# Optimization experiments

Measured on AMD Instinct MI355X. Metric: run time of the kernel, lower is better.

Reference implementation:

```python
import jax, jax.numpy as jnp
import numpy as np

B, L, HS, WS = 4, 5, 32, 32
C = 256            # dim == heads * dim_head
M, D = 8, 32       # heads, dim_head
T, R = 2, 4        # num_types, num_relations
I = M * D          # inner_dim
EPS = 1e-5


def setup_inputs() -> dict:
    key = jax.random.key(0)
    ks = jax.random.split(key, 12)
    w = 0.02
    x = jax.random.normal(ks[0], (B, L, HS, WS, C), dtype=jnp.float32)
    mask = jnp.ones((B, HS, WS, L, L), dtype=jnp.int32)
    prior_encoding = jax.random.randint(ks[1], (B, L, HS, WS, 3), 0, T).astype(jnp.float32)
    return {
        "x": x,
        "mask": mask,
        "prior_encoding": prior_encoding,
        "ln_w": jnp.ones((C,), jnp.float32),
        "ln_b": jnp.zeros((C,), jnp.float32),
        "Wq": jax.random.normal(ks[2], (T, C, I), jnp.float32) * w,
        "bq": jnp.zeros((T, I), jnp.float32),
        "Wk": jax.random.normal(ks[3], (T, C, I), jnp.float32) * w,
        "bk": jnp.zeros((T, I), jnp.float32),
        "Wv": jax.random.normal(ks[4], (T, C, I), jnp.float32) * w,
        "bv": jnp.zeros((T, I), jnp.float32),
        "Wa": jax.random.normal(ks[5], (T, I, C), jnp.float32) * w,
        "ba": jnp.zeros((T, C), jnp.float32),
        "rel_att": jax.random.normal(ks[6], (R, M, D, D), jnp.float32) * w,
        "rel_msg": jax.random.normal(ks[7], (R, M, D, D), jnp.float32) * w,
    }


def _hgt_forward(x, mask, prior_encoding, ln_w, ln_b, Wq, bq, Wk, bk, Wv, bv, Wa, ba, rel_att, rel_msg):
    # pre-LayerNorm over channel dim
    mu = jnp.mean(x, axis=-1, keepdims=True)
    var = jnp.mean(jnp.square(x - mu), axis=-1, keepdims=True)
    xn = (x - mu) * jax.lax.rsqrt(var + EPS) * ln_w + ln_b

    # [B,L,H,W,C] -> [B,H,W,L,C]
    xp = jnp.transpose(xn, (0, 2, 3, 1, 4))
    types = prior_encoding[:, :, 0, 0, 2].astype(jnp.int32)  # [B,L]

    # per-type q/k/v projections via gather of type-indexed weights
    q = jnp.einsum('bhwlc,blci->bhwli', xp, Wq[types]) + bq[types][:, None, None]
    k = jnp.einsum('bhwlc,blci->bhwli', xp, Wk[types]) + bk[types][:, None, None]
    v = jnp.einsum('bhwlc,blci->bhwli', xp, Wv[types]) + bv[types][:, None, None]

    def to_heads(t):  # [B,H,W,L,I] -> [B,M,H,W,L,D]
        return jnp.transpose(t.reshape(B, HS, WS, L, M, D), (0, 4, 1, 2, 3, 5))
    q, k, v = to_heads(q), to_heads(k), to_heads(v)

    # relation-indexed edge weights: e_type = t_i * T + t_j
    e = types[:, :, None] * T + types[:, None, :]              # [B,L,L]
    w_att = jnp.transpose(rel_att[e], (0, 3, 1, 2, 4, 5))      # [B,M,L,L,D,D]
    w_msg = jnp.transpose(rel_msg[e], (0, 3, 1, 2, 4, 5))

    scale = D ** -0.5
    q_w = jnp.einsum('bmhwip,bmijpq->bmhwijq', q, w_att)
    att = jnp.einsum('bmhwijq,bmhwjq->bmhwij', q_w, k) * scale
    att = jnp.where(mask[:, None] == 0, -1e9, att)
    att = jax.nn.softmax(att, axis=-1)

    v_msg = jnp.einsum('bmijpc,bmhwjp->bmhwijc', w_msg, v)
    out = jnp.einsum('bmhwij,bmhwijc->bmhwic', att, v_msg)

    # [B,M,H,W,L,D] -> [B,H,W,L,C]
    out = jnp.transpose(out, (0, 2, 3, 4, 1, 5)).reshape(B, HS, WS, L, I)
    out = jnp.einsum('bhwli,blic->bhwlc', out, Wa[types]) + ba[types][:, None, None]
    # dropout is identity at inference
    return jnp.transpose(out, (0, 3, 1, 2, 4))                 # [B,L,H,W,C]


def reference(x, mask, prior_encoding, ln_w, ln_b, Wq, bq, Wk, bk, Wv, bv, Wa, ba, rel_att, rel_msg):
    return _hgt_forward(x, mask, prior_encoding, ln_w, ln_b, Wq, bq, Wk, bk, Wv, bv, Wa, ba, rel_att, rel_msg)
```

## Files before the change

### kernel.cpp

```cpp
#include <hip/hip_runtime.h>
#include <hip/hip_bf16.h>
#include <math.h>

#define BB 4
#define LL 5
#define HSZ 32
#define WSZ 32
#define PP (HSZ*WSZ)
#define CC 256
#define MM 8
#define DD 32
#define II 256
#define TT 2
#define NTOK (BB*PP*LL*II)
#define TILE_ELEMS 8192
#define SCALE 0.17677669529663687f

typedef short bf16x8 __attribute__((ext_vector_type(8)));
typedef float f32x4 __attribute__((ext_vector_type(4)));

static __device__ __forceinline__ ushort f2bf(float f) {
    unsigned u = __float_as_uint(f);
    unsigned r = (u + 0x7fffu + ((u >> 16) & 1u)) >> 16;
    return (ushort)r;
}
static __device__ __forceinline__ float bf2f(ushort u) {
    return __uint_as_float(((unsigned)u) << 16);
}

__global__ __launch_bounds__(256) void k_fold(
    const float* __restrict__ Wq, const float* __restrict__ Wv,
    const float* __restrict__ Wk, const float* __restrict__ Wa,
    const float* __restrict__ bq, const float* __restrict__ bv,
    const float* __restrict__ rel_att, const float* __restrict__ rel_msg,
    const float* __restrict__ x,
    const float* __restrict__ lnw, const float* __restrict__ lnb,
    ushort* __restrict__ packW, float* __restrict__ bEff,
    ushort* __restrict__ xnPack)
{
    __shared__ float As[1024];
    __shared__ ushort Apack[8192];
    const int blk = blockIdx.x;
    const int tid = threadIdx.x;

    if (blk < 64) {
        const int p  = blk >> 5;
        const int t  = (blk >> 4) & 1;
        const int ts = (blk >> 3) & 1;
        const int m  = blk & 7;
        const float* A = (p == 0)
            ? rel_att + (size_t)((t * 2 + ts) * 8 + m) * 1024
            : rel_msg + (size_t)((ts * 2 + t) * 8 + m) * 1024;
        for (int i = tid; i < 1024; i += 256) As[i] = A[i];
        __syncthreads();

        const float* W = ((p == 0) ? Wq : Wv) + (size_t)t * 65536;
        const int k = tid;
        float wrow[32];
        #pragma unroll
        for (int u = 0; u < 8; ++u)
            *(float4*)&wrow[u * 4] = *(const float4*)&W[k * 256 + m * 32 + u * 4];

        const int slot = (p == 0 ? 0 : 4) + t * 2 + ts;
        ushort* base = packW + (size_t)slot * 65536;
        const int kt = k >> 5, j = k & 7, lq = ((k >> 3) & 3) * 16;
        #pragma unroll
        for (int q = 0; q < 32; ++q) {
            float acc = 0.f;
            #pragma unroll
            for (int pp = 0; pp < 32; ++pp) acc += wrow[pp] * As[pp * 32 + q];
            const int nt = m * 2 + (q >> 4);
            const int lane = lq + (q & 15);
            base[(size_t)((nt * 8 + kt) * 64 + lane) * 8 + j] = f2bf(acc);
        }
        if (tid < 32) {
            const int q = tid;
            const float* bi = ((p == 0) ? bq : bv) + t * 256 + m * 32;
            float acc = 0.f;
            #pragma unroll
            for (int pp = 0; pp < 32; ++pp) acc += bi[pp] * As[pp * 32 + q];
            bEff[(p ? 1024 : 0) + (t * 2 + ts) * 256 + m * 32 + q] = acc;
        }
    } else if (blk < 192) {
        const int idx = blk - 64;
        const int which = idx >> 6;
        const int gi = (idx & 63) * 256 + tid;
        const int t = gi >> 13;
        const int sub = gi & 8191;
        const float* src = ((which == 0) ? Wk : Wa) + (size_t)t * 65536;
        const int slot = (which == 0 ? 8 : 10) + t;
        const int nt = sub >> 9, kt = (sub >> 6) & 7, lane = sub & 63;
        const int k0 = kt * 32 + (lane >> 4) * 8;
        const int n  = nt * 16 + (lane & 15);
        ushort h[8];
        #pragma unroll
        for (int j = 0; j < 8; ++j) h[j] = f2bf(src[(size_t)(k0 + j) * 256 + n]);
        uint4 o;
        o.x = (unsigned)h[0] | ((unsigned)h[1] << 16);
        o.y = (unsigned)h[2] | ((unsigned)h[3] << 16);
        o.z = (unsigned)h[4] | ((unsigned)h[5] << 16);
        o.w = (unsigned)h[6] | ((unsigned)h[7] << 16);
        *(uint4*)(packW + (size_t)slot * 65536 + (size_t)sub * 8) = o;
    } else {
        const int lblk = blk - 192;
        const int bl  = lblk >> 5;
        const int pt  = lblk & 31;
        const int p0  = pt * 32;

        const int r  = tid >> 3;
        const int jj = tid & 7;
        const float* xrow = x + ((size_t)bl * PP + p0 + r) * CC;
        float4 xv[8];
        float s1 = 0.f, s2 = 0.f;
        #pragma unroll
        for (int u = 0; u < 8; ++u) {
            xv[u] = *(const float4*)(xrow + jj * 32 + u * 4);
            s1 += xv[u].x + xv[u].y + xv[u].z + xv[u].w;
            s2 += xv[u].x * xv[u].x + xv[u].y * xv[u].y + xv[u].z * xv[u].z + xv[u].w * xv[u].w;
        }
        s1 += __shfl_xor(s1, 1); s1 += __shfl_xor(s1, 2); s1 += __shfl_xor(s1, 4);
        s2 += __shfl_xor(s2, 1); s2 += __shfl_xor(s2, 2); s2 += __shfl_xor(s2, 4);
        const float mu   = s1 * (1.0f / 256.0f);
        const float var  = s2 * (1.0f / 256.0f) - mu * mu;
        const float rstd = rsqrtf(var + 1e-5f);

        const int mt_r = r >> 4, rm = r & 15;
        #pragma unroll
        for (int u = 0; u < 8; ++u) {
            const int c0 = jj * 32 + u * 4;
            const float4 g  = *(const float4*)(lnw + c0);
            const float4 bt = *(const float4*)(lnb + c0);
            const ushort h0 = f2bf((xv[u].x - mu) * rstd * g.x + bt.x);
            const ushort h1 = f2bf((xv[u].y - mu) * rstd * g.y + bt.y);
            const ushort h2 = f2bf((xv[u].z - mu) * rstd * g.z + bt.z);
            const ushort h3 = f2bf((xv[u].w - mu) * rstd * g.w + bt.w);
            uint2 w2;
            w2.x = (unsigned)h0 | ((unsigned)h1 << 16);
            w2.y = (unsigned)h2 | ((unsigned)h3 << 16);
            const int kt   = c0 >> 5;
            const int lsub = rm + (((c0 >> 3) & 3) << 4);
            const int j0   = c0 & 7;
            *(uint2*)&Apack[(((mt_r * 8 + kt) * 64 + lsub) << 3) + j0] = w2;
        }
        __syncthreads();

        const size_t tbase = (size_t)lblk * TILE_ELEMS;
        #pragma unroll
        for (int u = 0; u < 4; ++u) {
            const int ch = (tid + u * 256) * 8;
            *(uint4*)&xnPack[tbase + ch] = *(const uint4*)&Apack[ch];
        }
    }
}

__global__ __launch_bounds__(256) void k_proj(
    const ushort* __restrict__ xnPack, const float* __restrict__ prior,
    const ushort* __restrict__ packW, const float* __restrict__ bEff,
    const float* __restrict__ bk,
    ushort* __restrict__ qw0, ushort* __restrict__ qw1, ushort* __restrict__ kkO,
    ushort* __restrict__ vm0, ushort* __restrict__ vm1)
{
    __shared__ ushort As[8192];

    const int tid  = threadIdx.x;
    const int blk  = blockIdx.x;
    const int mat  = blk / 640;
    const int rem  = blk - mat * 640;
    const int bl   = rem >> 5;
    const int sub  = rem & 31;
    const int pg   = sub >> 1;
    const int half = sub & 1;
    const int t    = (int)prior[(size_t)bl * (PP * 3) + 2];

    int slot; const float* bias;
    if (mat < 2)       { slot = t * 2 + mat;           bias = bEff + slot * 256; }
    else if (mat == 2) { slot = 8 + t;                 bias = bk + t * 256; }
    else               { slot = 4 + t * 2 + (mat - 3); bias = bEff + 1024 + (t * 2 + (mat - 3)) * 256; }
    ushort* dst = (mat == 0) ? qw0 : (mat == 1) ? qw1 : (mat == 2) ? kkO : (mat == 3) ? vm0 : vm1;

    const int wv = tid >> 6, lane = tid & 63;

    const ushort* Bp = packW + (size_t)slot * 65536;
    bf16x8 bfr[8][2];
    #pragma unroll
    for (int kt = 0; kt < 8; ++kt)
        #pragma unroll
        for (int nn = 0; nn < 2; ++nn) {
            const int ntg = half * 8 + wv * 2 + nn;
            bfr[kt][nn] = *(const bf16x8*)&Bp[(size_t)((ntg * 8 + kt) * 64 + lane) * 8];
        }

    const int cl = lane & 15, rq = lane >> 4;
    const int colA = half * 128 + wv * 32 + cl;
    const int colB = colA + 16;
    const float biasA = bias[colA], biasB = bias[colB];

    #pragma unroll 1
    for (int tl = 0; tl < 2; ++tl) {
        const int pt = pg * 2 + tl;
        const size_t tbase = (size_t)(bl * 32 + pt) * TILE_ELEMS;
        __syncthreads();
        #pragma unroll
        for (int u = 0; u < 4; ++u) {
            const int ch = (tid + u * 256) * 8;
            *(uint4*)&As[ch] = *(const uint4*)&xnPack[tbase + ch];
        }
        __syncthreads();

        f32x4 acc[2][2];
        #pragma unroll
        for (int mt = 0; mt < 2; ++mt)
            #pragma unroll
            for (int nn = 0; nn < 2; ++nn)
                acc[mt][nn] = (f32x4){0.f, 0.f, 0.f, 0.f};

        #pragma unroll
        for (int kt = 0; kt < 8; ++kt) {
            const bf16x8 a0 = *(const bf16x8*)&As[((0 * 8 + kt) * 64 + lane) << 3];
            const bf16x8 a1 = *(const bf16x8*)&As[((1 * 8 + kt) * 64 + lane) << 3];
            acc[0][0] = __builtin_amdgcn_mfma_f32_16x16x32_bf16(a0, bfr[kt][0], acc[0][0], 0, 0, 0);
            acc[0][1] = __builtin_amdgcn_mfma_f32_16x16x32_bf16(a0, bfr[kt][1], acc[0][1], 0, 0, 0);
            acc[1][0] = __builtin_amdgcn_mfma_f32_16x16x32_bf16(a1, bfr[kt][0], acc[1][0], 0, 0, 0);
            acc[1][1] = __builtin_amdgcn_mfma_f32_16x16x32_bf16(a1, bfr[kt][1], acc[1][1], 0, 0, 0);
        }

        const int p0 = pt * 32;
        #pragma unroll
        for (int mt = 0; mt < 2; ++mt) {
            const int row0 = p0 + mt * 16 + rq * 4;
            #pragma unroll
            for (int r2 = 0; r2 < 4; ++r2) {
                const size_t rb = ((size_t)bl * PP + row0 + r2) * II;
                dst[rb + colA] = f2bf(acc[mt][0][r2] + biasA);
                dst[rb + colB] = f2bf(acc[mt][1][r2] + biasB);
            }
        }
    }
}

__global__ __launch_bounds__(256) void k_attn_lite(
    const ushort* __restrict__ qw0, const ushort* __restrict__ qw1,
    const ushort* __restrict__ kkI,
    const ushort* __restrict__ vm0, const ushort* __restrict__ vm1,
    const int* __restrict__ mask, const float* __restrict__ prior,
    ushort* __restrict__ aoPack)
{
    const int tid  = threadIdx.x;
    const int site = blockIdx.x * 4 + (tid >> 6);
    const int lane = tid & 63;
    const int b    = site >> 10;
    const int pix  = site & 1023;
    const int c0   = lane * 4;

    int ty[5];
    #pragma unroll
    for (int l = 0; l < 5; ++l)
        ty[l] = (int)prior[(size_t)(b * 5 + l) * (PP * 3) + 2];

    float qf[2][5][4], kf[5][4], vf[2][5][4];
    #pragma unroll
    for (int l = 0; l < 5; ++l) {
        const size_t base = (((size_t)(b * 5 + l) << 10) + pix) * II + c0;
        const ushort4 q0 = *(const ushort4*)(qw0 + base);
        const ushort4 q1 = *(const ushort4*)(qw1 + base);
        const ushort4 kv = *(const ushort4*)(kkI + base);
        const ushort4 v0 = *(const ushort4*)(vm0 + base);
        const ushort4 v1 = *(const ushort4*)(vm1 + base);
        qf[0][l][0] = bf2f(q0.x); qf[0][l][1] = bf2f(q0.y); qf[0][l][2] = bf2f(q0.z); qf[0][l][3] = bf2f(q0.w);
        qf[1][l][0] = bf2f(q1.x); qf[1][l][1] = bf2f(q1.y); qf[1][l][2] = bf2f(q1.z); qf[1][l][3] = bf2f(q1.w);
        kf[l][0]    = bf2f(kv.x); kf[l][1]    = bf2f(kv.y); kf[l][2]    = bf2f(kv.z); kf[l][3]    = bf2f(kv.w);
        vf[0][l][0] = bf2f(v0.x); vf[0][l][1] = bf2f(v0.y); vf[0][l][2] = bf2f(v0.z); vf[0][l][3] = bf2f(v0.w);
        vf[1][l][0] = bf2f(v1.x); vf[1][l][1] = bf2f(v1.y); vf[1][l][2] = bf2f(v1.z); vf[1][l][3] = bf2f(v1.w);
    }

    const int rr   = pix & 31;
    const int tile0 = b * 5 * 32 + (pix >> 5);
    const int mt   = rr >> 4;
    const int ktc  = c0 >> 5;
    const int lp   = (rr & 15) + 16 * ((c0 >> 3) & 3);
    const int j0   = c0 & 7;
    const int fofs = ((mt * 8 + ktc) * 64 + lp) * 8 + j0;

    #pragma unroll
    for (int i = 0; i < 5; ++i) {
        float lg[5];
        #pragma unroll
        for (int j = 0; j < 5; ++j) {
            const float s0 = qf[0][i][0] * kf[j][0] + qf[0][i][1] * kf[j][1]
                           + qf[0][i][2] * kf[j][2] + qf[0][i][3] * kf[j][3];
            const float s1 = qf[1][i][0] * kf[j][0] + qf[1][i][1] * kf[j][1]
                           + qf[1][i][2] * kf[j][2] + qf[1][i][3] * kf[j][3];
            float s = ty[j] ? s1 : s0;
            s += __shfl_xor(s, 1); s += __shfl_xor(s, 2); s += __shfl_xor(s, 4);
            const int mv = mask[((size_t)site * 5 + i) * 5 + j];
            lg[j] = mv ? s * SCALE : -1e9f;
        }
        float mx = lg[0];
        #pragma unroll
        for (int j = 1; j < 5; ++j) mx = fmaxf(mx, lg[j]);
        float ex[5], sum = 0.f;
        #pragma unroll
        for (int j = 0; j < 5; ++j) { ex[j] = __expf(lg[j] - mx); sum += ex[j]; }
        const float rs = 1.0f / sum;
        float o0 = 0.f, o1 = 0.f, o2 = 0.f, o3 = 0.f;
        #pragma unroll
        for (int j = 0; j < 5; ++j) {
            const float w = ex[j] * rs;
            o0 += w * (ty[i] ? vf[1][j][0] : vf[0][j][0]);
            o1 += w * (ty[i] ? vf[1][j][1] : vf[0][j][1]);
            o2 += w * (ty[i] ? vf[1][j][2] : vf[0][j][2]);
            o3 += w * (ty[i] ? vf[1][j][3] : vf[0][j][3]);
        }
        uint2 w2;
        w2.x = (unsigned)f2bf(o0) | ((unsigned)f2bf(o1) << 16);
        w2.y = (unsigned)f2bf(o2) | ((unsigned)f2bf(o3) << 16);
        *(uint2*)&aoPack[(size_t)(tile0 + i * 32) * TILE_ELEMS + fofs] = w2;
    }
}

__global__ __launch_bounds__(256) void k_out(
    const ushort* __restrict__ aoPack, const float* __restrict__ prior,
    const ushort* __restrict__ packW, const float* __restrict__ ba,
    float* __restrict__ out)
{
    __shared__ ushort As[8192];
    __shared__ float obufF[32 * 132];

    const int tid  = threadIdx.x;
    const int blk  = blockIdx.x;
    const int bl   = blk >> 6;
    const int sub  = blk & 63;
    const int pt   = sub >> 1;
    const int half = sub & 1;
    const int bbi  = bl / LL;
    const int l    = bl - bbi * LL;
    const int t    = (int)prior[(size_t)bl * (PP * 3) + 2];

    const int wv = tid >> 6, lane = tid & 63;
    const ushort* Bp = packW + (size_t)(10 + t) * 65536;
    bf16x8 bfr[8][2];
    #pragma unroll
    for (int kt = 0; kt < 8; ++kt)
        #pragma unroll
        for (int nn = 0; nn < 2; ++nn) {
            const int ntg = half * 8 + wv * 2 + nn;
            bfr[kt][nn] = *(const bf16x8*)&Bp[(size_t)((ntg * 8 + kt) * 64 + lane) * 8];
        }

    const size_t tbase = (size_t)(bl * 32 + pt) * TILE_ELEMS;
    #pragma unroll
    for (int u = 0; u < 4; ++u) {
        const int ch = (tid + u * 256) * 8;
        *(uint4*)&As[ch] = *(const uint4*)&aoPack[tbase + ch];
    }
    __syncthreads();

    const int cl = lane & 15, rq = lane >> 4;
    const int colL_A = wv * 32 + cl;
    const int colL_B = colL_A + 16;
    const float biasA = ba[t * CC + half * 128 + colL_A];
    const float biasB = ba[t * CC + half * 128 + colL_B];

    f32x4 acc[2][2];
    #pragma unroll
    for (int mt = 0; mt < 2; ++mt)
        #pragma unroll
        for (int nn = 0; nn < 2; ++nn)
            acc[mt][nn] = (f32x4){0.f, 0.f, 0.f, 0.f};

    #pragma unroll
    for (int kt = 0; kt < 8; ++kt) {
        const bf16x8 a0 = *(const bf16x8*)&As[((0 * 8 + kt) * 64 + lane) << 3];
        const bf16x8 a1 = *(const bf16x8*)&As[((1 * 8 + kt) * 64 + lane) << 3];
        acc[0][0] = __builtin_amdgcn_mfma_f32_16x16x32_bf16(a0, bfr[kt][0], acc[0][0], 0, 0, 0);
        acc[0][1] = __builtin_amdgcn_mfma_f32_16x16x32_bf16(a0, bfr[kt][1], acc[0][1], 0, 0, 0);
        acc[1][0] = __builtin_amdgcn_mfma_f32_16x16x32_bf16(a1, bfr[kt][0], acc[1][0], 0, 0, 0);
        acc[1][1] = __builtin_amdgcn_mfma_f32_16x16x32_bf16(a1, bfr[kt][1], acc[1][1], 0, 0, 0);
    }

    #pragma unroll
    for (int mt = 0; mt < 2; ++mt) {
        const int rowb = mt * 16 + rq * 4;
        #pragma unroll
        for (int r2 = 0; r2 < 4; ++r2) {
            obufF[(rowb + r2) * 132 + colL_A] = acc[mt][0][r2] + biasA;
            obufF[(rowb + r2) * 132 + colL_B] = acc[mt][1][r2] + biasB;
        }
    }
    __syncthreads();

    const int p0 = pt * 32;
    #pragma unroll
    for (int k2 = 0; k2 < 4; ++k2) {
        const int id  = tid + k2 * 256;
        const int row = id >> 5;
        const int ch  = (id & 31) * 4;
        const float4 v4 = *(const float4*)&obufF[row * 132 + ch];
        *(float4*)(out + ((size_t)(bbi * LL + l) * PP + p0 + row) * CC + half * 128 + ch) = v4;
    }
}

extern "C" void kernel_launch(void* const* d_in, const int* in_sizes, int n_in,
                              void* d_out, int out_size, void* d_ws, size_t ws_size,
                              hipStream_t stream) {
    const float* x       = (const float*)d_in[0];
    const int*   mask    = (const int*)d_in[1];
    const float* prior   = (const float*)d_in[2];
    const float* lnw     = (const float*)d_in[3];
    const float* lnb     = (const float*)d_in[4];
    const float* Wq      = (const float*)d_in[5];
    const float* bq      = (const float*)d_in[6];
    const float* Wk      = (const float*)d_in[7];
    const float* bk      = (const float*)d_in[8];
    const float* Wv      = (const float*)d_in[9];
    const float* bv      = (const float*)d_in[10];
    const float* Wa      = (const float*)d_in[11];
    const float* ba      = (const float*)d_in[12];
    const float* rel_att = (const float*)d_in[13];
    const float* rel_msg = (const float*)d_in[14];
    float* out = (float*)d_out;

    ushort* qw0    = (ushort*)d_ws;
    ushort* qw1    = qw0 + NTOK;
    ushort* kko    = qw1 + NTOK;
    ushort* vm0    = kko + NTOK;
    ushort* vm1    = vm0 + NTOK;
    ushort* aoPack = vm1 + NTOK;
    ushort* xnPack = aoPack + NTOK;
    ushort* packW  = xnPack + NTOK;
    float*  bEff   = (float*)(packW + 12 * 65536);

    hipLaunchKernelGGL(k_fold, dim3(832), dim3(256), 0, stream,
                       Wq, Wv, Wk, Wa, bq, bv, rel_att, rel_msg,
                       x, lnw, lnb, packW, bEff, xnPack);
    hipLaunchKernelGGL(k_proj, dim3(3200), dim3(256), 0, stream,
                       xnPack, prior, packW, bEff, bk, qw0, qw1, kko, vm0, vm1);
    hipLaunchKernelGGL(k_attn_lite, dim3(1024), dim3(256), 0, stream,
                       qw0, qw1, kko, vm0, vm1, mask, prior, aoPack);
    hipLaunchKernelGGL(k_out, dim3(1280), dim3(256), 0, stream,
                       aoPack, prior, packW, ba, out);
}
```

Measured before the change: 152.7 us.

## Fuse LayerNorm into projection kernel and loop over all five matrices per tile

LayerNorm and bf16 packing of x move out of the fold kernel into the projection kernel. Each projection block now normalizes its own 32-row tile into shared memory and loops over all five weight matrices, so the xnPack intermediate is no longer written to and read back from global memory. The grid shrinks from 3200 blocks to 1280. In exchange, each tile's LayerNorm is computed twice (once per column half), weight fragments are reloaded for every matrix, and the fold kernel no longer overlaps the LayerNorm work.

```diff
diff --git a/kernel.cpp b/kernel.cpp
--- a/kernel.cpp
+++ b/kernel.cpp
@@ -33,13 +33,9 @@
     const float* __restrict__ Wk, const float* __restrict__ Wa,
     const float* __restrict__ bq, const float* __restrict__ bv,
     const float* __restrict__ rel_att, const float* __restrict__ rel_msg,
-    const float* __restrict__ x,
-    const float* __restrict__ lnw, const float* __restrict__ lnb,
-    ushort* __restrict__ packW, float* __restrict__ bEff,
-    ushort* __restrict__ xnPack)
+    ushort* __restrict__ packW, float* __restrict__ bEff)
 {
     __shared__ float As[1024];
-    __shared__ ushort Apack[8192];
     const int blk = blockIdx.x;
     const int tid = threadIdx.x;
 
@@ -81,7 +77,7 @@
             for (int pp = 0; pp < 32; ++pp) acc += bi[pp] * As[pp * 32 + q];
             bEff[(p ? 1024 : 0) + (t * 2 + ts) * 256 + m * 32 + q] = acc;
         }
-    } else if (blk < 192) {
+    } else {
         const int idx = blk - 64;
         const int which = idx >> 6;
         const int gi = (idx & 63) * 256 + tid;
@@ -101,12 +97,29 @@
         o.z = (unsigned)h[4] | ((unsigned)h[5] << 16);
         o.w = (unsigned)h[6] | ((unsigned)h[7] << 16);
         *(uint4*)(packW + (size_t)slot * 65536 + (size_t)sub * 8) = o;
-    } else {
-        const int lblk = blk - 192;
-        const int bl  = lblk >> 5;
-        const int pt  = lblk & 31;
-        const int p0  = pt * 32;
-
+    }
+}
+
+__global__ __launch_bounds__(256) void k_proj(
+    const float* __restrict__ x, const float* __restrict__ lnw,
+    const float* __restrict__ lnb, const float* __restrict__ prior,
+    const ushort* __restrict__ packW, const float* __restrict__ bEff,
+    const float* __restrict__ bk,
+    ushort* __restrict__ qw0, ushort* __restrict__ qw1, ushort* __restrict__ kkO,
+    ushort* __restrict__ vm0, ushort* __restrict__ vm1)
+{
+    __shared__ ushort As[8192];
+
+    const int tid  = threadIdx.x;
+    const int blk  = blockIdx.x;
+    const int bl   = blk >> 6;
+    const int rem  = blk & 63;
+    const int pt   = rem >> 1;
+    const int half = rem & 1;
+    const int p0   = pt * 32;
+    const int t    = (int)prior[(size_t)bl * (PP * 3) + 2];
+
+    {
         const int r  = tid >> 3;
         const int jj = tid & 7;
         const float* xrow = x + ((size_t)bl * PP + p0 + r) * CC;
@@ -140,72 +153,33 @@
             const int kt   = c0 >> 5;
             const int lsub = rm + (((c0 >> 3) & 3) << 4);
             const int j0   = c0 & 7;
-            *(uint2*)&Apack[(((mt_r * 8 + kt) * 64 + lsub) << 3) + j0] = w2;
-        }
-        __syncthreads();
-
-        const size_t tbase = (size_t)lblk * TILE_ELEMS;
-        #pragma unroll
-        for (int u = 0; u < 4; ++u) {
-            const int ch = (tid + u * 256) * 8;
-            *(uint4*)&xnPack[tbase + ch] = *(const uint4*)&Apack[ch];
-        }
-    }
-}
-
-__global__ __launch_bounds__(256) void k_proj(
-    const ushort* __restrict__ xnPack, const float* __restrict__ prior,
-    const ushort* __restrict__ packW, const float* __restrict__ bEff,
-    const float* __restrict__ bk,
-    ushort* __restrict__ qw0, ushort* __restrict__ qw1, ushort* __restrict__ kkO,
-    ushort* __restrict__ vm0, ushort* __restrict__ vm1)
-{
-    __shared__ ushort As[8192];
-
-    const int tid  = threadIdx.x;
-    const int blk  = blockIdx.x;
-    const int mat  = blk / 640;
-    const int rem  = blk - mat * 640;
-    const int bl   = rem >> 5;
-    const int sub  = rem & 31;
-    const int pg   = sub >> 1;
-    const int half = sub & 1;
-    const int t    = (int)prior[(size_t)bl * (PP * 3) + 2];
-
-    int slot; const float* bias;
-    if (mat < 2)       { slot = t * 2 + mat;           bias = bEff + slot * 256; }
-    else if (mat == 2) { slot = 8 + t;                 bias = bk + t * 256; }
-    else               { slot = 4 + t * 2 + (mat - 3); bias = bEff + 1024 + (t * 2 + (mat - 3)) * 256; }
-    ushort* dst = (mat == 0) ? qw0 : (mat == 1) ? qw1 : (mat == 2) ? kkO : (mat == 3) ? vm0 : vm1;
+            *(uint2*)&As[(((mt_r * 8 + kt) * 64 + lsub) << 3) + j0] = w2;
+        }
+    }
+    __syncthreads();
 
     const int wv = tid >> 6, lane = tid & 63;
-
-    const ushort* Bp = packW + (size_t)slot * 65536;
-    bf16x8 bfr[8][2];
-    #pragma unroll
-    for (int kt = 0; kt < 8; ++kt)
-        #pragma unroll
-        for (int nn = 0; nn < 2; ++nn) {
-            const int ntg = half * 8 + wv * 2 + nn;
-            bfr[kt][nn] = *(const bf16x8*)&Bp[(size_t)((ntg * 8 + kt) * 64 + lane) * 8];
-        }
-
     const int cl = lane & 15, rq = lane >> 4;
     const int colA = half * 128 + wv * 32 + cl;
     const int colB = colA + 16;
-    const float biasA = bias[colA], biasB = bias[colB];
 
     #pragma unroll 1
-    for (int tl = 0; tl < 2; ++tl) {
-        const int pt = pg * 2 + tl;
-        const size_t tbase = (size_t)(bl * 32 + pt) * TILE_ELEMS;
-        __syncthreads();
-        #pragma unroll
-        for (int u = 0; u < 4; ++u) {
-            const int ch = (tid + u * 256) * 8;
-            *(uint4*)&As[ch] = *(const uint4*)&xnPack[tbase + ch];
-        }
-        __syncthreads();
+    for (int mat = 0; mat < 5; ++mat) {
+        int slot; const float* bias;
+        if (mat < 2)       { slot = t * 2 + mat;           bias = bEff + slot * 256; }
+        else if (mat == 2) { slot = 8 + t;                 bias = bk + t * 256; }
+        else               { slot = 4 + t * 2 + (mat - 3); bias = bEff + 1024 + (t * 2 + (mat - 3)) * 256; }
+        ushort* dst = (mat == 0) ? qw0 : (mat == 1) ? qw1 : (mat == 2) ? kkO : (mat == 3) ? vm0 : vm1;
+
+        const ushort* Bp = packW + (size_t)slot * 65536;
+        bf16x8 bfr[8][2];
+        #pragma unroll
+        for (int kt = 0; kt < 8; ++kt)
+            #pragma unroll
+            for (int nn = 0; nn < 2; ++nn) {
+                const int ntg = half * 8 + wv * 2 + nn;
+                bfr[kt][nn] = *(const bf16x8*)&Bp[(size_t)((ntg * 8 + kt) * 64 + lane) * 8];
+            }
 
         f32x4 acc[2][2];
         #pragma unroll
@@ -224,7 +198,7 @@
             acc[1][1] = __builtin_amdgcn_mfma_f32_16x16x32_bf16(a1, bfr[kt][1], acc[1][1], 0, 0, 0);
         }
 
-        const int p0 = pt * 32;
+        const float biasA = bias[colA], biasB = bias[colB];
         #pragma unroll
         for (int mt = 0; mt < 2; ++mt) {
             const int row0 = p0 + mt * 16 + rq * 4;
@@ -426,15 +400,14 @@
     ushort* vm0    = kko + NTOK;
     ushort* vm1    = vm0 + NTOK;
     ushort* aoPack = vm1 + NTOK;
-    ushort* xnPack = aoPack + NTOK;
-    ushort* packW  = xnPack + NTOK;
+    ushort* packW  = aoPack + NTOK;
     float*  bEff   = (float*)(packW + 12 * 65536);
 
-    hipLaunchKernelGGL(k_fold, dim3(832), dim3(256), 0, stream,
+    hipLaunchKernelGGL(k_fold, dim3(192), dim3(256), 0, stream,
                        Wq, Wv, Wk, Wa, bq, bv, rel_att, rel_msg,
-                       x, lnw, lnb, packW, bEff, xnPack);
-    hipLaunchKernelGGL(k_proj, dim3(3200), dim3(256), 0, stream,
-                       xnPack, prior, packW, bEff, bk, qw0, qw1, kko, vm0, vm1);
+                       packW, bEff);
+    hipLaunchKernelGGL(k_proj, dim3(1280), dim3(256), 0, stream,
+                       x, lnw, lnb, prior, packW, bEff, bk, qw0, qw1, kko, vm0, vm1);
     hipLaunchKernelGGL(k_attn_lite, dim3(1024), dim3(256), 0, stream,
                        qw0, qw1, kko, vm0, vm1, mask, prior, aoPack);
     hipLaunchKernelGGL(k_out, dim3(1280), dim3(256), 0, stream,
```

Result: slower. 182.7 us (+19.7%).

## Write attention output row-major and load MFMA A fragments directly from global

Applied to the files above, without the earlier changes.

The attention kernel now writes its output in plain row-major token layout instead of a pre-swizzled MFMA tile layout. The output projection loads A fragments straight from global memory, dropping its LDS staging buffer and a barrier. Inside the attention kernel, mask loads are made wave-uniform and hoisted, all logits are computed before the shuffle reductions so the shuffles can be batched, V loads are deferred, and per-row type selects become branches with normalization applied once at the end. The cost is less coalesced, strided global reads for A in k_out (16-byte loads with a 512-byte row stride).

```diff
diff --git a/kernel.cpp b/kernel.cpp
--- a/kernel.cpp
+++ b/kernel.cpp
@@ -238,12 +238,12 @@
     }
 }
 
-__global__ __launch_bounds__(256) void k_attn_lite(
+__global__ __launch_bounds__(256) void k_attn(
     const ushort* __restrict__ qw0, const ushort* __restrict__ qw1,
     const ushort* __restrict__ kkI,
     const ushort* __restrict__ vm0, const ushort* __restrict__ vm1,
     const int* __restrict__ mask, const float* __restrict__ prior,
-    ushort* __restrict__ aoPack)
+    ushort* __restrict__ ao)
 {
     const int tid  = threadIdx.x;
     const int site = blockIdx.x * 4 + (tid >> 6);
@@ -252,78 +252,109 @@
     const int pix  = site & 1023;
     const int c0   = lane * 4;
 
+    const int usite = __builtin_amdgcn_readfirstlane(site);
+    const int ub    = usite >> 10;
+
     int ty[5];
     #pragma unroll
     for (int l = 0; l < 5; ++l)
-        ty[l] = (int)prior[(size_t)(b * 5 + l) * (PP * 3) + 2];
-
-    float qf[2][5][4], kf[5][4], vf[2][5][4];
+        ty[l] = (int)prior[(size_t)(ub * 5 + l) * (PP * 3) + 2];
+
+    int mv[5][5];
+    #pragma unroll
+    for (int i = 0; i < 5; ++i)
+        #pragma unroll
+        for (int j = 0; j < 5; ++j)
+            mv[i][j] = mask[(size_t)usite * 25 + i * 5 + j];
+
+    float qf[2][5][4], kf[5][4];
     #pragma unroll
     for (int l = 0; l < 5; ++l) {
         const size_t base = (((size_t)(b * 5 + l) << 10) + pix) * II + c0;
         const ushort4 q0 = *(const ushort4*)(qw0 + base);
         const ushort4 q1 = *(const ushort4*)(qw1 + base);
         const ushort4 kv = *(const ushort4*)(kkI + base);
-        const ushort4 v0 = *(const ushort4*)(vm0 + base);
-        const ushort4 v1 = *(const ushort4*)(vm1 + base);
         qf[0][l][0] = bf2f(q0.x); qf[0][l][1] = bf2f(q0.y); qf[0][l][2] = bf2f(q0.z); qf[0][l][3] = bf2f(q0.w);
         qf[1][l][0] = bf2f(q1.x); qf[1][l][1] = bf2f(q1.y); qf[1][l][2] = bf2f(q1.z); qf[1][l][3] = bf2f(q1.w);
         kf[l][0]    = bf2f(kv.x); kf[l][1]    = bf2f(kv.y); kf[l][2]    = bf2f(kv.z); kf[l][3]    = bf2f(kv.w);
+    }
+
+    float s[5][5];
+    #pragma unroll
+    for (int j = 0; j < 5; ++j) {
+        if (ty[j]) {
+            #pragma unroll
+            for (int i = 0; i < 5; ++i)
+                s[i][j] = qf[1][i][0] * kf[j][0] + qf[1][i][1] * kf[j][1]
+                        + qf[1][i][2] * kf[j][2] + qf[1][i][3] * kf[j][3];
+        } else {
+            #pragma unroll
+            for (int i = 0; i < 5; ++i)
+                s[i][j] = qf[0][i][0] * kf[j][0] + qf[0][i][1] * kf[j][1]
+                        + qf[0][i][2] * kf[j][2] + qf[0][i][3] * kf[j][3];
+        }
+    }
+    #pragma unroll
+    for (int i = 0; i < 5; ++i)
+        #pragma unroll
+        for (int j = 0; j < 5; ++j) s[i][j] += __shfl_xor(s[i][j], 1);
+    #pragma unroll
+    for (int i = 0; i < 5; ++i)
+        #pragma unroll
+        for (int j = 0; j < 5; ++j) s[i][j] += __shfl_xor(s[i][j], 2);
+    #pragma unroll
+    for (int i = 0; i < 5; ++i)
+        #pragma unroll
+        for (int j = 0; j < 5; ++j) s[i][j] += __shfl_xor(s[i][j], 4);
+
+    float vf[2][5][4];
+    #pragma unroll
+    for (int l = 0; l < 5; ++l) {
+        const size_t base = (((size_t)(b * 5 + l) << 10) + pix) * II + c0;
+        const ushort4 v0 = *(const ushort4*)(vm0 + base);
+        const ushort4 v1 = *(const ushort4*)(vm1 + base);
         vf[0][l][0] = bf2f(v0.x); vf[0][l][1] = bf2f(v0.y); vf[0][l][2] = bf2f(v0.z); vf[0][l][3] = bf2f(v0.w);
         vf[1][l][0] = bf2f(v1.x); vf[1][l][1] = bf2f(v1.y); vf[1][l][2] = bf2f(v1.z); vf[1][l][3] = bf2f(v1.w);
     }
 
-    const int rr   = pix & 31;
-    const int tile0 = b * 5 * 32 + (pix >> 5);
-    const int mt   = rr >> 4;
-    const int ktc  = c0 >> 5;
-    const int lp   = (rr & 15) + 16 * ((c0 >> 3) & 3);
-    const int j0   = c0 & 7;
-    const int fofs = ((mt * 8 + ktc) * 64 + lp) * 8 + j0;
-
     #pragma unroll
     for (int i = 0; i < 5; ++i) {
         float lg[5];
         #pragma unroll
-        for (int j = 0; j < 5; ++j) {
-            const float s0 = qf[0][i][0] * kf[j][0] + qf[0][i][1] * kf[j][1]
-                           + qf[0][i][2] * kf[j][2] + qf[0][i][3] * kf[j][3];
-            const float s1 = qf[1][i][0] * kf[j][0] + qf[1][i][1] * kf[j][1]
-                           + qf[1][i][2] * kf[j][2] + qf[1][i][3] * kf[j][3];
-            float s = ty[j] ? s1 : s0;
-            s += __shfl_xor(s, 1); s += __shfl_xor(s, 2); s += __shfl_xor(s, 4);
-            const int mv = mask[((size_t)site * 5 + i) * 5 + j];
-            lg[j] = mv ? s * SCALE : -1e9f;
-        }
-        float mx = lg[0];
-        #pragma unroll
-        for (int j = 1; j < 5; ++j) mx = fmaxf(mx, lg[j]);
+        for (int j = 0; j < 5; ++j)
+            lg[j] = mv[i][j] ? s[i][j] * SCALE : -1e9f;
+        const float mx = fmaxf(fmaxf(fmaxf(lg[0], lg[1]), fmaxf(lg[2], lg[3])), lg[4]);
         float ex[5], sum = 0.f;
         #pragma unroll
         for (int j = 0; j < 5; ++j) { ex[j] = __expf(lg[j] - mx); sum += ex[j]; }
         const float rs = 1.0f / sum;
         float o0 = 0.f, o1 = 0.f, o2 = 0.f, o3 = 0.f;
-        #pragma unroll
-        for (int j = 0; j < 5; ++j) {
-            const float w = ex[j] * rs;
-            o0 += w * (ty[i] ? vf[1][j][0] : vf[0][j][0]);
-            o1 += w * (ty[i] ? vf[1][j][1] : vf[0][j][1]);
-            o2 += w * (ty[i] ? vf[1][j][2] : vf[0][j][2]);
-            o3 += w * (ty[i] ? vf[1][j][3] : vf[0][j][3]);
-        }
+        if (ty[i]) {
+            #pragma unroll
+            for (int j = 0; j < 5; ++j) {
+                o0 += ex[j] * vf[1][j][0]; o1 += ex[j] * vf[1][j][1];
+                o2 += ex[j] * vf[1][j][2]; o3 += ex[j] * vf[1][j][3];
+            }
+        } else {
+            #pragma unroll
+            for (int j = 0; j < 5; ++j) {
+                o0 += ex[j] * vf[0][j][0]; o1 += ex[j] * vf[0][j][1];
+                o2 += ex[j] * vf[0][j][2]; o3 += ex[j] * vf[0][j][3];
+            }
+        }
+        o0 *= rs; o1 *= rs; o2 *= rs; o3 *= rs;
         uint2 w2;
         w2.x = (unsigned)f2bf(o0) | ((unsigned)f2bf(o1) << 16);
         w2.y = (unsigned)f2bf(o2) | ((unsigned)f2bf(o3) << 16);
-        *(uint2*)&aoPack[(size_t)(tile0 + i * 32) * TILE_ELEMS + fofs] = w2;
+        *(uint2*)&ao[(((size_t)(b * 5 + i) << 10) + pix) * II + c0] = w2;
     }
 }
 
 __global__ __launch_bounds__(256) void k_out(
-    const ushort* __restrict__ aoPack, const float* __restrict__ prior,
+    const ushort* __restrict__ ao, const float* __restrict__ prior,
     const ushort* __restrict__ packW, const float* __restrict__ ba,
     float* __restrict__ out)
 {
-    __shared__ ushort As[8192];
     __shared__ float obufF[32 * 132];
 
     const int tid  = threadIdx.x;
@@ -347,13 +378,10 @@
             bfr[kt][nn] = *(const bf16x8*)&Bp[(size_t)((ntg * 8 + kt) * 64 + lane) * 8];
         }
 
-    const size_t tbase = (size_t)(bl * 32 + pt) * TILE_ELEMS;
-    #pragma unroll
-    for (int u = 0; u < 4; ++u) {
-        const int ch = (tid + u * 256) * 8;
-        *(uint4*)&As[ch] = *(const uint4*)&aoPack[tbase + ch];
-    }
-    __syncthreads();
+    const int p0   = pt * 32;
+    const int rowA = lane & 15;
+    const int ksub = (lane >> 4) * 8;
+    const ushort* a_base = ao + ((size_t)(bl * PP + p0 + rowA)) * II + ksub;
 
     const int cl = lane & 15, rq = lane >> 4;
     const int colL_A = wv * 32 + cl;
@@ -370,8 +398,8 @@
 
     #pragma unroll
     for (int kt = 0; kt < 8; ++kt) {
-        const bf16x8 a0 = *(const bf16x8*)&As[((0 * 8 + kt) * 64 + lane) << 3];
-        const bf16x8 a1 = *(const bf16x8*)&As[((1 * 8 + kt) * 64 + lane) << 3];
+        const bf16x8 a0 = *(const bf16x8*)(a_base + kt * 32);
+        const bf16x8 a1 = *(const bf16x8*)(a_base + (size_t)16 * II + kt * 32);
         acc[0][0] = __builtin_amdgcn_mfma_f32_16x16x32_bf16(a0, bfr[kt][0], acc[0][0], 0, 0, 0);
         acc[0][1] = __builtin_amdgcn_mfma_f32_16x16x32_bf16(a0, bfr[kt][1], acc[0][1], 0, 0, 0);
         acc[1][0] = __builtin_amdgcn_mfma_f32_16x16x32_bf16(a1, bfr[kt][0], acc[1][0], 0, 0, 0);
@@ -389,7 +417,6 @@
     }
     __syncthreads();
 
-    const int p0 = pt * 32;
     #pragma unroll
     for (int k2 = 0; k2 < 4; ++k2) {
         const int id  = tid + k2 * 256;
@@ -425,8 +452,8 @@
     ushort* kko    = qw1 + NTOK;
     ushort* vm0    = kko + NTOK;
     ushort* vm1    = vm0 + NTOK;
-    ushort* aoPack = vm1 + NTOK;
-    ushort* xnPack = aoPack + NTOK;
+    ushort* ao     = vm1 + NTOK;
+    ushort* xnPack = ao + NTOK;
     ushort* packW  = xnPack + NTOK;
     float*  bEff   = (float*)(packW + 12 * 65536);
 
@@ -435,8 +462,8 @@
                        x, lnw, lnb, packW, bEff, xnPack);
     hipLaunchKernelGGL(k_proj, dim3(3200), dim3(256), 0, stream,
                        xnPack, prior, packW, bEff, bk, qw0, qw1, kko, vm0, vm1);
-    hipLaunchKernelGGL(k_attn_lite, dim3(1024), dim3(256), 0, stream,
-                       qw0, qw1, kko, vm0, vm1, mask, prior, aoPack);
+    hipLaunchKernelGGL(k_attn, dim3(1024), dim3(256), 0, stream,
+                       qw0, qw1, kko, vm0, vm1, mask, prior, ao);
     hipLaunchKernelGGL(k_out, dim3(1280), dim3(256), 0, stream,
-                       aoPack, prior, packW, ba, out);
-}
+                       ao, prior, packW, ba, out);
+}
```

Measured after the change: 154.9 us. No clear change (+1.5%).
